# Optimization experiments

Hardware: AMD Instinct MI355X
Metric: run time of the kernel (lower is better)

The kernel has to match this reference:

```python
import jax, jax.numpy as jnp
import numpy as np

HEADS = 8
KS = 7
PAD = 3


def grouped_conv1x1(x, w):
    # x: (B, Cin, H, W), w: (heads, Cout/h, Cin/h) -> (B, Cout, H, W)
    B, Cin, H, W = x.shape
    g, co, ci = w.shape
    xg = x.reshape(B, g, ci, H, W)
    out = jnp.einsum('bgchw,goc->bgohw', xg, w)
    return out.reshape(B, g * co, H, W)


def unfold2d(p, k):
    # p: (B, C, Hp, Wp) -> (B, C, H, W, k, k) sliding windows, stride 1
    B, C, Hp, Wp = p.shape
    H, W = Hp - k + 1, Wp - k + 1
    rows = [jnp.stack([p[:, :, i:i + H, j:j + W] for j in range(k)], axis=-1)
            for i in range(k)]
    return jnp.stack(rows, axis=-2)  # (B,C,H,W,k,k)


def setup_inputs() -> dict:
    key = jax.random.key(0)
    ks = jax.random.split(key, 7)
    B, Cin, H, W = 8, 64, 64, 64
    Cout = 64
    g = HEADS
    return {
        'x': jax.random.normal(ks[0], (B, Cin, H, W), jnp.float32),
        'r': jax.random.normal(ks[1], (1,), jnp.float32),
        'w_q': jax.random.normal(ks[2], (g, Cout // g, Cin // g), jnp.float32) * 0.2,
        'w_k': jax.random.normal(ks[3], (g, Cout // g, Cin // g), jnp.float32) * 0.2,
        'w_v': jax.random.normal(ks[4], (g, Cout // g, Cin // g), jnp.float32) * 0.2,
        'rel_h': jax.random.normal(ks[5], (Cout // 2, KS), jnp.float32),
        'rel_w': jax.random.normal(ks[6], (Cout // 2, KS), jnp.float32),
    }


def reference(x, r, w_q, w_k, w_v, rel_h, rel_w):
    B, Cin, H, W = x.shape
    g = HEADS
    Cout = w_q.shape[0] * w_q.shape[1]
    dh = Cout // g

    padded = jnp.pad(x, ((0, 0), (0, 0), (PAD, PAD), (PAD, PAD)))
    q = grouped_conv1x1(x, w_q)            # (B, Cout, H, W)
    k = grouped_conv1x1(padded, w_k)       # (B, Cout, H+2p, W+2p)
    v = grouped_conv1x1(padded, w_v)

    k = unfold2d(k, KS)                    # (B, Cout, H, W, KS, KS)
    v = unfold2d(v, KS)

    # learnable relative positional encoding: split channels in half,
    # add rel_h along window-height, rel_w along window-width
    half = Cout // 2
    k_h = k[:, :half] + rel_h[None, :, None, None, :, None]
    k_w = k[:, half:] + rel_w[None, :, None, None, None, :]
    k = jnp.concatenate([k_h, k_w], axis=1)

    K2 = KS * KS
    k = k.reshape(B, g, dh, H, W, K2)
    v = v.reshape(B, g, dh, H, W, K2)
    q = q.reshape(B, g, dh, H, W, 1)

    scale = np.sqrt(g / Cout).astype(np.float32)
    logits = (q * k).sum(axis=2, keepdims=True) * scale   # (B,g,1,H,W,K2)
    attn = jax.nn.softmax(logits, axis=-1)
    out = (attn * v).sum(axis=-1)                          # (B,g,dh,H,W)
    return out.reshape(B, Cout, H, W)
```

## Files before the change

kernel.cpp:

```cpp
#include <hip/hip_runtime.h>
#include <math.h>

#define NG  8
#define DH  8
#define NCP 4
#define KS  7
#define PAD 3
#define TH  16
#define TW  32
#define OW  2
#define TPH 22
#define RSTW 40
#define PLW  (TPH * RSTW)
#define CH  64
#define HH  64
#define WW  64

typedef __fp16 h2v __attribute__((ext_vector_type(2)));
typedef __fp16 h4v __attribute__((ext_vector_type(4)));

__device__ __forceinline__ int imin(int a, int b) { return a < b ? a : b; }
__device__ __forceinline__ int imax(int a, int b) { return a > b ? a : b; }

__global__ __launch_bounds__(256, 1)
void saconv_kernel(const float* __restrict__ x,
                   const float* __restrict__ wq,
                   const float* __restrict__ wk,
                   const float* __restrict__ wv,
                   const float* __restrict__ relh,
                   const float* __restrict__ relw,
                   float* __restrict__ out) {
  __shared__ h2v xs2[NCP * PLW];
  __shared__ float swq[DH * DH];
  __shared__ float swk[DH * DH];
  __shared__ float swv[DH * DH];
  __shared__ float srel[DH * KS];

  const int tx  = threadIdx.x;
  const int ty  = threadIdx.y;
  const int tid = ty * 16 + tx;
  const int bz  = blockIdx.z;
  const int b   = bz >> 3;
  const int g   = bz & 7;
  const int h0  = blockIdx.y * TH;
  const int w0  = blockIdx.x * TW;

  if (tid < DH * DH) swq[tid] = wq[g * DH * DH + tid];
  else if (tid < 2 * DH * DH) swk[tid - 64] = wk[g * DH * DH + tid - 64];
  else if (tid < 3 * DH * DH) swv[tid - 128] = wv[g * DH * DH + tid - 128];
  else if (tid < 3 * DH * DH + DH * KS) {
    int t2 = tid - 192;
    int c = t2 / KS, t = t2 - c * KS;
    int gc = g * DH + c;
    srel[t2] = (g < 4) ? relh[gc * KS + t] : relw[(gc - 32) * KS + t];
  }

  const float* xb = x + (size_t)(b * CH + g * DH) * (HH * WW);
  const int NCHK = NCP * TPH * 19;
  #pragma unroll
  for (int kk = 0; kk < 7; kk++) {
    int f = tid + kk * 256;
    if (f < NCHK) {
      int cp  = f / (TPH * 19);
      int r   = f - cp * (TPH * 19);
      int row = r / 19;
      int cc  = r - row * 19;
      int yy  = h0 + row - PAD;
      int cy  = imin(imax(yy, 0), HH - 1);
      bool yok = (yy >= 0) & (yy < HH);
      const float* p0 = xb + ((size_t)(2 * cp) * HH + cy) * WW;
      float v0[2], v1[2];
      #pragma unroll
      for (int e = 0; e < 2; e++) {
        int xx = w0 + 2 * cc + e - PAD;
        int cx = imin(imax(xx, 0), WW - 1);
        bool inb = yok & (xx >= 0) & (xx < WW);
        float a0 = p0[cx];
        float a1 = p0[HH * WW + cx];
        v0[e] = inb ? a0 : 0.0f;
        v1[e] = inb ? a1 : 0.0f;
      }
      h2v pk0 = __builtin_amdgcn_cvt_pkrtz(v0[0], v1[0]);
      h2v pk1 = __builtin_amdgcn_cvt_pkrtz(v0[1], v1[1]);
      h4v w4 = { pk0.x, pk0.y, pk1.x, pk1.y };
      *(h4v*)&xs2[cp * PLW + row * RSTW + 2 * cc] = w4;
    }
  }
  __syncthreads();

  const float scale = 0.35355339059327373f;
  const float L2E   = 1.4426950408889634f;
  h2v  qkh[OW][NCP];
  float rq[OW][KS];
  {
    float xc[OW][DH];
    #pragma unroll
    for (int o = 0; o < OW; o++)
      #pragma unroll
      for (int cp = 0; cp < NCP; cp++) {
        h2v wv2 = xs2[cp * PLW + (ty + PAD) * RSTW + (2 * tx + o + PAD)];
        xc[o][2 * cp]     = (float)wv2.x;
        xc[o][2 * cp + 1] = (float)wv2.y;
      }
    float q_[OW][DH];
    #pragma unroll
    for (int o = 0; o < OW; o++)
      #pragma unroll
      for (int c = 0; c < DH; c++) {
        float a = 0.f;
        #pragma unroll
        for (int ci = 0; ci < DH; ci++)
          a = fmaf(swq[c * DH + ci], xc[o][ci], a);
        q_[o][c] = a;
      }
    #pragma unroll
    for (int o = 0; o < OW; o++)
      #pragma unroll
      for (int cp = 0; cp < NCP; cp++) {
        float a0 = 0.f, a1 = 0.f;
        #pragma unroll
        for (int c = 0; c < DH; c++) {
          a0 = fmaf(q_[o][c], swk[c * DH + 2 * cp], a0);
          a1 = fmaf(q_[o][c], swk[c * DH + 2 * cp + 1], a1);
        }
        qkh[o][cp] = __builtin_amdgcn_cvt_pkrtz(a0 * (scale * L2E), a1 * (scale * L2E));
      }
    #pragma unroll
    for (int o = 0; o < OW; o++)
      #pragma unroll
      for (int t = 0; t < KS; t++) {
        float a = 0.f;
        #pragma unroll
        for (int c = 0; c < DH; c++)
          a = fmaf(q_[o][c], srel[c * KS + t], a);
        rq[o][t] = a * (scale * L2E);
      }
  }

  const bool useI = (g < 4);

  float s[OW], xa[OW][DH];
  #pragma unroll
  for (int o = 0; o < OW; o++) {
    s[o] = 0.f;
    #pragma unroll
    for (int ci = 0; ci < DH; ci++) xa[o][ci] = 0.f;
  }

  #pragma unroll
  for (int i = 0; i < KS; i++) {
    const int wbase = (ty + i) * RSTW + 2 * tx;
    h2v xw[NCP][8];
    #pragma unroll
    for (int cp = 0; cp < NCP; cp++) {
      const h4v* bp = (const h4v*)&xs2[cp * PLW + wbase];
      h4v r0 = bp[0], r1 = bp[1], r2 = bp[2], r3 = bp[3];
      xw[cp][0] = __builtin_shufflevector(r0, r0, 0, 1);
      xw[cp][1] = __builtin_shufflevector(r0, r0, 2, 3);
      xw[cp][2] = __builtin_shufflevector(r1, r1, 0, 1);
      xw[cp][3] = __builtin_shufflevector(r1, r1, 2, 3);
      xw[cp][4] = __builtin_shufflevector(r2, r2, 0, 1);
      xw[cp][5] = __builtin_shufflevector(r2, r2, 2, 3);
      xw[cp][6] = __builtin_shufflevector(r3, r3, 0, 1);
      xw[cp][7] = __builtin_shufflevector(r3, r3, 2, 3);
    }

    #pragma unroll
    for (int o = 0; o < OW; o++) {
      float e[KS];
      float se = 0.f;
      #pragma unroll
      for (int j = 0; j < KS; j++) {
        float d = useI ? rq[o][i] : rq[o][j];
        #pragma unroll
        for (int cp = 0; cp < NCP; cp++)
          d = __builtin_amdgcn_fdot2(qkh[o][cp], xw[cp][o + j], d, false);
        e[j] = exp2f(d);
        se += e[j];
      }
      s[o] += se;
      #pragma unroll
      for (int cp = 0; cp < NCP; cp++) {
        float a0 = xa[o][2 * cp];
        float a1 = xa[o][2 * cp + 1];
        #pragma unroll
        for (int j = 0; j < KS; j++) {
          a0 = fmaf(e[j], (float)xw[cp][o + j].x, a0);
          a1 = fmaf(e[j], (float)xw[cp][o + j].y, a1);
        }
        xa[o][2 * cp]     = a0;
        xa[o][2 * cp + 1] = a1;
      }
    }
  }

  #pragma unroll
  for (int o = 0; o < OW; o++) {
    float inv = 1.0f / s[o];
    #pragma unroll
    for (int ci = 0; ci < DH; ci++) xa[o][ci] *= inv;
  }

  const int h = h0 + ty;
  const int wbase = w0 + 2 * tx;
  #pragma unroll
  for (int c = 0; c < DH; c++) {
    float2 v2;
    {
      float a0 = 0.f, a1 = 0.f;
      #pragma unroll
      for (int ci = 0; ci < DH; ci++) {
        a0 = fmaf(swv[c * DH + ci], xa[0][ci], a0);
        a1 = fmaf(swv[c * DH + ci], xa[1][ci], a1);
      }
      v2.x = a0; v2.y = a1;
    }
    *(float2*)(&out[((size_t)(b * CH + g * DH + c) * HH + h) * WW + wbase]) = v2;
  }
}

extern "C" void kernel_launch(void* const* d_in, const int* in_sizes, int n_in,
                              void* d_out, int out_size, void* d_ws, size_t ws_size,
                              hipStream_t stream) {
  const float* x    = (const float*)d_in[0];
  const float* wq   = (const float*)d_in[2];
  const float* wk   = (const float*)d_in[3];
  const float* wv   = (const float*)d_in[4];
  const float* relh = (const float*)d_in[5];
  const float* relw = (const float*)d_in[6];
  float* out = (float*)d_out;

  const int B = in_sizes[0] / (CH * HH * WW);
  dim3 grid(WW / TW, HH / TH, B * NG);
  dim3 block(16, 16, 1);
  saconv_kernel<<<grid, block, 0, stream>>>(x, wq, wk, wv, relh, relw, out);
}
```

Before: 19.67 us.

## Split 7-row attention window across two thread halves and reduce via shuffles

```diff
diff --git a/kernel.cpp b/kernel.cpp
--- a/kernel.cpp
+++ b/kernel.cpp
@@ -10,7 +10,7 @@
 #define TW  32
 #define OW  2
 #define TPH 22
-#define RSTW 40
+#define RSTW 42
 #define PLW  (TPH * RSTW)
 #define CH  64
 #define HH  64
@@ -22,7 +22,7 @@
 __device__ __forceinline__ int imin(int a, int b) { return a < b ? a : b; }
 __device__ __forceinline__ int imax(int a, int b) { return a > b ? a : b; }
 
-__global__ __launch_bounds__(256, 1)
+__global__ __launch_bounds__(512, 2)
 void saconv_kernel(const float* __restrict__ x,
                    const float* __restrict__ wq,
                    const float* __restrict__ wk,
@@ -36,9 +36,10 @@
   __shared__ float swv[DH * DH];
   __shared__ float srel[DH * KS];
 
-  const int tx  = threadIdx.x;
-  const int ty  = threadIdx.y;
-  const int tid = ty * 16 + tx;
+  const int tx    = threadIdx.x;
+  const int ihalf = threadIdx.y;
+  const int ty    = threadIdx.z;
+  const int tid   = tx + 16 * ihalf + 32 * ty;
   const int bz  = blockIdx.z;
   const int b   = bz >> 3;
   const int g   = bz & 7;
@@ -58,9 +59,9 @@
   const float* xb = x + (size_t)(b * CH + g * DH) * (HH * WW);
   const int NCHK = NCP * TPH * 19;
   #pragma unroll
-  for (int kk = 0; kk < 7; kk++) {
-    int f = tid + kk * 256;
-    if (f < NCHK) {
+  for (int kk = 0; kk < 4; kk++) {
+    int f = tid + kk * 512;
+    if (kk < 3 || f < NCHK) {
       int cp  = f / (TPH * 19);
       int r   = f - cp * (TPH * 19);
       int row = r / 19;
@@ -91,7 +92,7 @@
   const float scale = 0.35355339059327373f;
   const float L2E   = 1.4426950408889634f;
   h2v  qkh[OW][NCP];
-  float rq[OW][KS];
+  float rq[OW][8];
   {
     float xc[OW][DH];
     #pragma unroll
@@ -126,7 +127,7 @@
         qkh[o][cp] = __builtin_amdgcn_cvt_pkrtz(a0 * (scale * L2E), a1 * (scale * L2E));
       }
     #pragma unroll
-    for (int o = 0; o < OW; o++)
+    for (int o = 0; o < OW; o++) {
       #pragma unroll
       for (int t = 0; t < KS; t++) {
         float a = 0.f;
@@ -135,87 +136,108 @@
           a = fmaf(q_[o][c], srel[c * KS + t], a);
         rq[o][t] = a * (scale * L2E);
       }
+      rq[o][7] = 0.f;
+    }
   }
 
   const bool useI = (g < 4);
-
-  float s[OW], xa[OW][DH];
+  float s[OW] = {0.f, 0.f};
+  float xa[OW][DH];
+  #pragma unroll
+  for (int o = 0; o < OW; o++)
+    #pragma unroll
+    for (int ci = 0; ci < DH; ci++) xa[o][ci] = 0.f;
+
+  #pragma unroll
+  for (int u = 0; u < 4; u++) {
+    if (u < 3 || ihalf == 0) {
+      const int row = ty + 4 * ihalf + u;
+      const int wbase = row * RSTW + 2 * tx;
+      h2v xw[NCP][8];
+      #pragma unroll
+      for (int cp = 0; cp < NCP; cp++) {
+        const h4v* bp = (const h4v*)&xs2[cp * PLW + wbase];
+        h4v r0 = bp[0], r1 = bp[1], r2 = bp[2], r3 = bp[3];
+        xw[cp][0] = __builtin_shufflevector(r0, r0, 0, 1);
+        xw[cp][1] = __builtin_shufflevector(r0, r0, 2, 3);
+        xw[cp][2] = __builtin_shufflevector(r1, r1, 0, 1);
+        xw[cp][3] = __builtin_shufflevector(r1, r1, 2, 3);
+        xw[cp][4] = __builtin_shufflevector(r2, r2, 0, 1);
+        xw[cp][5] = __builtin_shufflevector(r2, r2, 2, 3);
+        xw[cp][6] = __builtin_shufflevector(r3, r3, 0, 1);
+        xw[cp][7] = __builtin_shufflevector(r3, r3, 2, 3);
+      }
+
+      #pragma unroll
+      for (int o = 0; o < OW; o++) {
+        float e[KS];
+        float se = 0.f;
+        #pragma unroll
+        for (int j = 0; j < KS; j++) {
+          float d = useI ? (ihalf ? rq[o][u + 4] : rq[o][u]) : rq[o][j];
+          #pragma unroll
+          for (int cp = 0; cp < NCP; cp++)
+            d = __builtin_amdgcn_fdot2(qkh[o][cp], xw[cp][o + j], d, false);
+          e[j] = exp2f(d);
+          se += e[j];
+        }
+        s[o] += se;
+        #pragma unroll
+        for (int cp = 0; cp < NCP; cp++) {
+          float a0 = xa[o][2 * cp];
+          float a1 = xa[o][2 * cp + 1];
+          #pragma unroll
+          for (int j = 0; j < KS; j++) {
+            a0 = fmaf(e[j], (float)xw[cp][o + j].x, a0);
+            a1 = fmaf(e[j], (float)xw[cp][o + j].y, a1);
+          }
+          xa[o][2 * cp]     = a0;
+          xa[o][2 * cp + 1] = a1;
+        }
+      }
+    }
+  }
+
+  float xav[OW][DH];
+  float inv[OW];
   #pragma unroll
   for (int o = 0; o < OW; o++) {
-    s[o] = 0.f;
-    #pragma unroll
-    for (int ci = 0; ci < DH; ci++) xa[o][ci] = 0.f;
-  }
-
-  #pragma unroll
-  for (int i = 0; i < KS; i++) {
-    const int wbase = (ty + i) * RSTW + 2 * tx;
-    h2v xw[NCP][8];
-    #pragma unroll
-    for (int cp = 0; cp < NCP; cp++) {
-      const h4v* bp = (const h4v*)&xs2[cp * PLW + wbase];
-      h4v r0 = bp[0], r1 = bp[1], r2 = bp[2], r3 = bp[3];
-      xw[cp][0] = __builtin_shufflevector(r0, r0, 0, 1);
-      xw[cp][1] = __builtin_shufflevector(r0, r0, 2, 3);
-      xw[cp][2] = __builtin_shufflevector(r1, r1, 0, 1);
-      xw[cp][3] = __builtin_shufflevector(r1, r1, 2, 3);
-      xw[cp][4] = __builtin_shufflevector(r2, r2, 0, 1);
-      xw[cp][5] = __builtin_shufflevector(r2, r2, 2, 3);
-      xw[cp][6] = __builtin_shufflevector(r3, r3, 0, 1);
-      xw[cp][7] = __builtin_shufflevector(r3, r3, 2, 3);
-    }
-
-    #pragma unroll
-    for (int o = 0; o < OW; o++) {
-      float e[KS];
-      float se = 0.f;
-      #pragma unroll
-      for (int j = 0; j < KS; j++) {
-        float d = useI ? rq[o][i] : rq[o][j];
-        #pragma unroll
-        for (int cp = 0; cp < NCP; cp++)
-          d = __builtin_amdgcn_fdot2(qkh[o][cp], xw[cp][o + j], d, false);
-        e[j] = exp2f(d);
-        se += e[j];
-      }
-      s[o] += se;
-      #pragma unroll
-      for (int cp = 0; cp < NCP; cp++) {
-        float a0 = xa[o][2 * cp];
-        float a1 = xa[o][2 * cp + 1];
-        #pragma unroll
-        for (int j = 0; j < KS; j++) {
-          a0 = fmaf(e[j], (float)xw[cp][o + j].x, a0);
-          a1 = fmaf(e[j], (float)xw[cp][o + j].y, a1);
-        }
-        xa[o][2 * cp]     = a0;
-        xa[o][2 * cp + 1] = a1;
-      }
-    }
-  }
-
-  #pragma unroll
-  for (int o = 0; o < OW; o++) {
-    float inv = 1.0f / s[o];
-    #pragma unroll
-    for (int ci = 0; ci < DH; ci++) xa[o][ci] *= inv;
-  }
+    float st = s[o] + __shfl_xor(s[o], 16, 64);
+    inv[o] = 1.0f / st;
+  }
+  #pragma unroll
+  for (int o = 0; o < OW; o++)
+    #pragma unroll
+    for (int ci = 0; ci < DH; ci++) {
+      float t_ = xa[o][ci];
+      xav[o][ci] = (t_ + __shfl_xor(t_, 16, 64)) * inv[o];
+    }
 
   const int h = h0 + ty;
   const int wbase = w0 + 2 * tx;
-  #pragma unroll
-  for (int c = 0; c < DH; c++) {
-    float2 v2;
-    {
+  float* ob = out + (((size_t)(b * CH + g * DH) * HH + h) * WW + wbase);
+  if (ihalf == 0) {
+    #pragma unroll
+    for (int n = 0; n < 4; n++) {
       float a0 = 0.f, a1 = 0.f;
       #pragma unroll
       for (int ci = 0; ci < DH; ci++) {
-        a0 = fmaf(swv[c * DH + ci], xa[0][ci], a0);
-        a1 = fmaf(swv[c * DH + ci], xa[1][ci], a1);
-      }
-      v2.x = a0; v2.y = a1;
-    }
-    *(float2*)(&out[((size_t)(b * CH + g * DH + c) * HH + h) * WW + wbase]) = v2;
+        a0 = fmaf(swv[n * DH + ci], xav[0][ci], a0);
+        a1 = fmaf(swv[n * DH + ci], xav[1][ci], a1);
+      }
+      *(float2*)(ob + (size_t)n * (HH * WW)) = make_float2(a0, a1);
+    }
+  } else {
+    #pragma unroll
+    for (int n = 0; n < 4; n++) {
+      float a0 = 0.f, a1 = 0.f;
+      #pragma unroll
+      for (int ci = 0; ci < DH; ci++) {
+        a0 = fmaf(swv[(4 + n) * DH + ci], xav[0][ci], a0);
+        a1 = fmaf(swv[(4 + n) * DH + ci], xav[1][ci], a1);
+      }
+      *(float2*)(ob + (size_t)(4 + n) * (HH * WW)) = make_float2(a0, a1);
+    }
   }
 }
 
@@ -232,6 +254,6 @@
 
   const int B = in_sizes[0] / (CH * HH * WW);
   dim3 grid(WW / TW, HH / TH, B * NG);
-  dim3 block(16, 16, 1);
+  dim3 block(16, 2, 16);
   saconv_kernel<<<grid, block, 0, stream>>>(x, wq, wk, wv, relh, relw, out);
 }
```

New measurement: 21.21 us. 1.08x slower.
